# Performance work log

Measured on AMD Instinct MI355X. Metric: run time of the kernel, lower is better.

The kernel has to match this reference:

```python
import jax, jax.numpy as jnp
import numpy as np

C = 128
IC = C // 2  # inter_channels
EPS = 1e-5   # InstanceNorm2d default eps (affine=False -> no learned scale/shift)


def setup_inputs() -> dict:
    key = jax.random.key(0)
    ks = jax.random.split(key, 9)
    s = 0.05
    return {
        "x": jax.random.normal(ks[0], (4, C, 64, 64), dtype=jnp.float32),
        "g_w": jax.random.normal(ks[1], (IC, C), dtype=jnp.float32) * s,
        "g_b": jax.random.normal(ks[2], (IC,), dtype=jnp.float32) * s,
        "theta_w": jax.random.normal(ks[3], (IC, C), dtype=jnp.float32) * s,
        "theta_b": jax.random.normal(ks[4], (IC,), dtype=jnp.float32) * s,
        "phi_w": jax.random.normal(ks[5], (IC, C), dtype=jnp.float32) * s,
        "phi_b": jax.random.normal(ks[6], (IC,), dtype=jnp.float32) * s,
        "W_w": jax.random.normal(ks[7], (C, IC), dtype=jnp.float32) * s,
        "W_b": jax.random.normal(ks[8], (C,), dtype=jnp.float32) * s,
    }


def reference(x, g_w, g_b, theta_w, theta_b, phi_w, phi_b, W_w, W_b):
    B, Cc, H, Wd = x.shape
    N = H * Wd
    xf = x.reshape(B, Cc, N)  # [B, C, N]

    def proj(w, b):  # 1x1 conv == channel matmul
        return jnp.einsum('oc,bcn->bon', w, xf) + b[:, None]  # [B, IC, N]

    g_x = proj(g_w, g_b).transpose(0, 2, 1)        # [B, N, IC]
    theta_x = proj(theta_w, theta_b).transpose(0, 2, 1)  # [B, N, IC]
    phi_x = proj(phi_w, phi_b)                     # [B, IC, N]

    f = jnp.einsum('bnc,bcm->bnm', theta_x, phi_x)  # [B, N, N] unscaled affinity
    f = jax.nn.softmax(f, axis=-1)
    y = jnp.einsum('bnm,bmc->bnc', f, g_x)          # [B, N, IC]
    y = y.transpose(0, 2, 1)                        # [B, IC, N]

    W_y = jnp.einsum('oc,bcn->bon', W_w, y) + W_b[:, None]  # [B, C, N]
    # InstanceNorm2d (affine=False): normalize per (batch, channel) over spatial
    mean = W_y.mean(axis=-1, keepdims=True)
    var = W_y.var(axis=-1, keepdims=True)
    W_y = (W_y - mean) * jax.lax.rsqrt(var + EPS)

    return x + W_y.reshape(B, Cc, H, Wd)
```

## Files before the change

kernel.cpp:

```cpp
#include <hip/hip_runtime.h>

typedef __attribute__((ext_vector_type(4))) float f32x4;
typedef __attribute__((ext_vector_type(8))) short s16x8;
typedef __attribute__((ext_vector_type(4))) short s16x4;
typedef __attribute__((ext_vector_type(4))) unsigned int u32x4;

#define NB 4
#define CH 128
#define ICH 64
#define NSP 4096
#define KSPLIT 8
#define SEGK 512
#define LDK 72
#define LDW 136

static __device__ __forceinline__ unsigned short f2bf(float f) {
  unsigned int u = __builtin_bit_cast(unsigned int, f);
  u += 0x7fffu + ((u >> 16) & 1u);
  return (unsigned short)(u >> 16);
}

__global__ __launch_bounds__(256) void k_proj(
    const float* __restrict__ x,
    const float* __restrict__ gw, const float* __restrict__ gbias,
    const float* __restrict__ tw, const float* __restrict__ tbias,
    const float* __restrict__ pw, const float* __restrict__ pbias,
    unsigned short* __restrict__ thetaT, unsigned short* __restrict__ phiT,
    unsigned short* __restrict__ gout)
{
  __shared__ __align__(16) float sxf[CH * 65];
  __shared__ __align__(16) unsigned short sW[ICH * LDW];
  const int b = blockIdx.y, z = blockIdx.z;
  const int n0 = blockIdx.x * 64;
  const int t = threadIdx.x;
  const float* Wz = (z == 0) ? tw : (z == 1) ? pw : gw;
  const float* Bz = (z == 0) ? tbias : (z == 1) ? pbias : gbias;
  const float* xb = x + (size_t)b * CH * NSP;
#pragma unroll
  for (int i = 0; i < 8; ++i) {
    int idx = t + 256 * i;
    int c = idx >> 4, ch = idx & 15;
    *(float4*)(sxf + c * 65 + ch * 4) = *(const float4*)(xb + (size_t)c * NSP + n0 + ch * 4);
  }
#pragma unroll
  for (int i = 0; i < 8; ++i) {
    int idx = t + 256 * i;
    int o = idx >> 5, col = (idx & 31) * 4;
    float4 wv = *(const float4*)(Wz + o * CH + col);
    unsigned int p0 = (unsigned int)f2bf(wv.x) | ((unsigned int)f2bf(wv.y) << 16);
    unsigned int p1 = (unsigned int)f2bf(wv.z) | ((unsigned int)f2bf(wv.w) << 16);
    *(unsigned int*)(&sW[o * LDW + col]) = p0;
    *(unsigned int*)(&sW[o * LDW + col + 2]) = p1;
  }
  __syncthreads();

  const int wave = t >> 6, lane = t & 63;
  const int l15 = lane & 15, quad = lane >> 4;
  const int nw = wave * 16;
  s16x8 aq[4];
#pragma unroll
  for (int kc = 0; kc < 4; ++kc) {
#pragma unroll
    for (int j = 0; j < 8; ++j)
      aq[kc][j] = (short)f2bf(sxf[(kc * 32 + quad * 8 + j) * 65 + nw + l15]);
  }
  __syncthreads();

  unsigned short* ldsT = (unsigned short*)sxf;

#pragma unroll
  for (int osub = 0; osub < 4; ++osub) {
    f32x4 acc = (f32x4){0.f, 0.f, 0.f, 0.f};
#pragma unroll
    for (int kc = 0; kc < 4; ++kc) {
      const unsigned short* wp = &sW[(osub * 16 + l15) * LDW + kc * 32 + quad * 8];
      s16x4 lo = *(const s16x4*)(wp);
      s16x4 hi = *(const s16x4*)(wp + 4);
      s16x8 bw = __builtin_shufflevector(lo, hi, 0, 1, 2, 3, 4, 5, 6, 7);
      acc = __builtin_amdgcn_mfma_f32_16x16x32_bf16(aq[kc], bw, acc, 0, 0, 0);
    }
    float bv = Bz[osub * 16 + l15];
    if (z < 2) {
      unsigned short* outp = (z == 0) ? thetaT : phiT;
#pragma unroll
      for (int r = 0; r < 4; ++r)
        outp[((size_t)b * NSP + n0 + nw + quad * 4 + r) * ICH + osub * 16 + l15] =
            f2bf(acc[r] + bv);
    } else {
#pragma unroll
      for (int r = 0; r < 4; ++r)
        ldsT[(nw + quad * 4 + r) * LDK + osub * 16 + l15] = f2bf(acc[r] + bv);
    }
  }
  if (z == 2) {
    __syncthreads();
    int o = t >> 2, chunk = t & 3;
    unsigned short vv[16];
#pragma unroll
    for (int jj = 0; jj < 16; ++jj) vv[jj] = ldsT[(chunk * 16 + jj) * LDK + o];
    unsigned int words[8];
#pragma unroll
    for (int i = 0; i < 8; ++i)
      words[i] = (unsigned int)vv[2 * i] | ((unsigned int)vv[2 * i + 1] << 16);
    unsigned short* gp = gout + ((size_t)b * ICH + o) * NSP + n0 + chunk * 16;
    *(u32x4*)(gp) = (u32x4){words[0], words[1], words[2], words[3]};
    *(u32x4*)(gp + 8) = (u32x4){words[4], words[5], words[6], words[7]};
  }
}

__global__ __launch_bounds__(128, 2) void k_attn(
    const unsigned short* __restrict__ thetaT,
    const unsigned short* __restrict__ phiT,
    const unsigned short* __restrict__ gmat,
    float* __restrict__ Opart, float* __restrict__ lpart)
{
  __shared__ unsigned short ldsK[64 * LDK];
  __shared__ unsigned short ldsV[64 * LDK];
  __shared__ unsigned short ldsP[2][64 * LDK];
  const int qt = blockIdx.x, b = blockIdx.y, seg = blockIdx.z;
  const int t = threadIdx.x;
  const int wave = t >> 6, lane = t & 63;
  const int l15 = lane & 15, quad = lane >> 4;
  const int q0 = qt * 128 + wave * 64;

  s16x8 aq[4][2];
  const unsigned short* th = thetaT + ((size_t)b * NSP + q0) * ICH;
#pragma unroll
  for (int qs = 0; qs < 4; ++qs)
#pragma unroll
    for (int ks = 0; ks < 2; ++ks)
      aq[qs][ks] = __builtin_bit_cast(s16x8,
          *(const u32x4*)(th + (qs * 16 + l15) * ICH + ks * 32 + quad * 8));

  f32x4 Oacc[4][4];
  float lacc[4][4];
#pragma unroll
  for (int i = 0; i < 4; ++i)
#pragma unroll
    for (int j = 0; j < 4; ++j) { Oacc[i][j] = (f32x4){0.f, 0.f, 0.f, 0.f}; lacc[i][j] = 0.f; }

  const unsigned short* ph = phiT + (size_t)b * NSP * ICH;
  const unsigned short* gb = gmat + (size_t)b * ICH * NSP;
  const int k0 = seg * SEGK;

  for (int kt = 0; kt < SEGK / 64; ++kt) {
    const int key0 = k0 + kt * 64;
    __syncthreads();
#pragma unroll
    for (int i = 0; i < 4; ++i) {
      int idx = t + 128 * i;
      int row = idx >> 3, c16 = idx & 7;
      *(u32x4*)(&ldsK[row * LDK + c16 * 8]) =
          *(const u32x4*)(ph + (size_t)(key0 + row) * ICH + c16 * 8);
      *(u32x4*)(&ldsV[row * LDK + c16 * 8]) =
          *(const u32x4*)(gb + (size_t)row * NSP + key0 + c16 * 8);
    }
    __syncthreads();

    s16x8 bk[4][2];
#pragma unroll
    for (int kc = 0; kc < 4; ++kc)
#pragma unroll
      for (int ks = 0; ks < 2; ++ks)
        bk[kc][ks] = *(const s16x8*)(&ldsK[(kc * 16 + l15) * LDK + ks * 32 + quad * 8]);

    unsigned short* myP = &ldsP[wave][0];
#pragma unroll
    for (int qs = 0; qs < 4; ++qs) {
      f32x4 s[4];
#pragma unroll
      for (int kc = 0; kc < 4; ++kc) {
        f32x4 acc = (f32x4){0.f, 0.f, 0.f, 0.f};
        acc = __builtin_amdgcn_mfma_f32_16x16x32_bf16(aq[qs][0], bk[kc][0], acc, 0, 0, 0);
        acc = __builtin_amdgcn_mfma_f32_16x16x32_bf16(aq[qs][1], bk[kc][1], acc, 0, 0, 0);
        s[kc] = acc;
      }
      float tmp[4] = {0.f, 0.f, 0.f, 0.f};
#pragma unroll
      for (int kc = 0; kc < 4; ++kc)
#pragma unroll
        for (int r = 0; r < 4; ++r) {
          float e = __expf(s[kc][r]);
          s[kc][r] = e;
          tmp[r] += e;
        }
#pragma unroll
      for (int m = 1; m < 16; m <<= 1)
#pragma unroll
        for (int r = 0; r < 4; ++r) tmp[r] += __shfl_xor(tmp[r], m, 64);
#pragma unroll
      for (int r = 0; r < 4; ++r) lacc[qs][r] += tmp[r];
#pragma unroll
      for (int kc = 0; kc < 4; ++kc)
#pragma unroll
        for (int r = 0; r < 4; ++r)
          myP[(qs * 16 + quad * 4 + r) * LDK + kc * 16 + l15] = f2bf(s[kc][r]);
    }

    s16x8 bv[2][4];
#pragma unroll
    for (int ks = 0; ks < 2; ++ks)
#pragma unroll
      for (int ds = 0; ds < 4; ++ds)
        bv[ks][ds] = *(const s16x8*)(&ldsV[(ds * 16 + l15) * LDK + ks * 32 + quad * 8]);
#pragma unroll
    for (int qs = 0; qs < 4; ++qs)
#pragma unroll
      for (int ks = 0; ks < 2; ++ks) {
        s16x8 ap2 = *(const s16x8*)(&myP[(qs * 16 + l15) * LDK + ks * 32 + quad * 8]);
#pragma unroll
        for (int ds = 0; ds < 4; ++ds)
          Oacc[qs][ds] = __builtin_amdgcn_mfma_f32_16x16x32_bf16(ap2, bv[ks][ds], Oacc[qs][ds], 0, 0, 0);
      }
  }

  float* Ob = Opart + (((size_t)seg * NB + b) * NSP + q0) * ICH;
#pragma unroll
  for (int qs = 0; qs < 4; ++qs)
#pragma unroll
    for (int ds = 0; ds < 4; ++ds)
#pragma unroll
      for (int r = 0; r < 4; ++r)
        Ob[(qs * 16 + quad * 4 + r) * ICH + ds * 16 + l15] = Oacc[qs][ds][r];
  if (l15 == 0) {
    float* lb = lpart + ((size_t)seg * NB + b) * NSP + q0;
#pragma unroll
    for (int qs = 0; qs < 4; ++qs)
#pragma unroll
      for (int r = 0; r < 4; ++r)
        lb[qs * 16 + quad * 4 + r] = lacc[qs][r];
  }
}

__global__ __launch_bounds__(256) void k_combine(
    const float* __restrict__ Opart, const float* __restrict__ lpart,
    unsigned short* __restrict__ y)
{
  int idx = blockIdx.x * 256 + threadIdx.x;
  int d = idx & 63;
  int q = (idx >> 6) & (NSP - 1);
  int b = idx >> 18;
  float o = 0.f, l = 0.f;
#pragma unroll
  for (int s = 0; s < KSPLIT; ++s) {
    o += Opart[(((size_t)s * NB + b) * NSP + q) * ICH + d];
    l += lpart[((size_t)s * NB + b) * NSP + q];
  }
  y[idx] = f2bf(o / l);
}

__global__ __launch_bounds__(256) void k_wy(
    const unsigned short* __restrict__ y,
    const float* __restrict__ Ww,
    float* __restrict__ WyT, float* __restrict__ stat)
{
  const int b = blockIdx.y;
  const int nt = blockIdx.x;
  const int t = threadIdx.x;
  const int wave = t >> 6, lane = t & 63;
  const int l15 = lane & 15, quad = lane >> 4;
  s16x8 bw[8][2];
#pragma unroll
  for (int cc = 0; cc < 8; ++cc)
#pragma unroll
    for (int ks = 0; ks < 2; ++ks) {
      const float* wp = Ww + (cc * 16 + l15) * ICH + ks * 32 + quad * 8;
      s16x8 e;
#pragma unroll
      for (int j = 0; j < 8; ++j) e[j] = (short)f2bf(wp[j]);
      bw[cc][ks] = e;
    }
  float sums[8], sq[8];
#pragma unroll
  for (int cc = 0; cc < 8; ++cc) { sums[cc] = 0.f; sq[cc] = 0.f; }
  const unsigned short* yb = y + (size_t)b * NSP * ICH;
#pragma unroll
  for (int ns = 0; ns < 4; ++ns) {
    const int n0 = nt * 256 + wave * 64 + ns * 16;
    s16x8 ay[2];
#pragma unroll
    for (int ks = 0; ks < 2; ++ks)
      ay[ks] = __builtin_bit_cast(s16x8,
          *(const u32x4*)(yb + (size_t)(n0 + l15) * ICH + ks * 32 + quad * 8));
#pragma unroll
    for (int cc = 0; cc < 8; ++cc) {
      f32x4 acc = (f32x4){0.f, 0.f, 0.f, 0.f};
      acc = __builtin_amdgcn_mfma_f32_16x16x32_bf16(ay[0], bw[cc][0], acc, 0, 0, 0);
      acc = __builtin_amdgcn_mfma_f32_16x16x32_bf16(ay[1], bw[cc][1], acc, 0, 0, 0);
      float* wout = WyT + (size_t)(b * NSP + n0 + quad * 4) * CH + cc * 16 + l15;
#pragma unroll
      for (int r = 0; r < 4; ++r) {
        float v = acc[r];
        sums[cc] += v;
        sq[cc] += v * v;
        wout[r * CH] = v;
      }
    }
  }
#pragma unroll
  for (int cc = 0; cc < 8; ++cc) {
    sums[cc] += __shfl_xor(sums[cc], 16, 64);
    sums[cc] += __shfl_xor(sums[cc], 32, 64);
    sq[cc] += __shfl_xor(sq[cc], 16, 64);
    sq[cc] += __shfl_xor(sq[cc], 32, 64);
  }
  if (quad == 0) {
#pragma unroll
    for (int cc = 0; cc < 8; ++cc) {
      atomicAdd(&stat[(b * CH + cc * 16 + l15) * 2 + 0], sums[cc]);
      atomicAdd(&stat[(b * CH + cc * 16 + l15) * 2 + 1], sq[cc]);
    }
  }
}

__global__ __launch_bounds__(256) void k_norm(
    const float* __restrict__ WyT, const float* __restrict__ stat,
    const float* __restrict__ x, float* __restrict__ out)
{
  __shared__ float sWy[32 * 132];
  const int nt = blockIdx.x;
  const int b = blockIdx.y;
  const int t = threadIdx.x;
  const int n0 = nt * 32;
#pragma unroll
  for (int i = 0; i < 4; ++i) {
    int idx = t + 256 * i;
    int row = idx >> 5, c4 = idx & 31;
    *(float4*)(&sWy[row * 132 + c4 * 4]) =
        *(const float4*)(WyT + (size_t)(b * NSP + n0 + row) * CH + c4 * 4);
  }
  __syncthreads();
#pragma unroll
  for (int j = 0; j < 4; ++j) {
    int u = t + 256 * j;
    int co = u >> 3, nq = u & 7;
    float s = stat[(b * CH + co) * 2 + 0];
    float ss = stat[(b * CH + co) * 2 + 1];
    float mean = s * (1.f / NSP);
    float var = ss * (1.f / NSP) - mean * mean;
    float rs = rsqrtf(var + 1e-5f);
    float4 xv = *(const float4*)(x + (size_t)(b * CH + co) * NSP + n0 + nq * 4);
    float4 ov;
    ov.x = xv.x + (sWy[(nq * 4 + 0) * 132 + co] - mean) * rs;
    ov.y = xv.y + (sWy[(nq * 4 + 1) * 132 + co] - mean) * rs;
    ov.z = xv.z + (sWy[(nq * 4 + 2) * 132 + co] - mean) * rs;
    ov.w = xv.w + (sWy[(nq * 4 + 3) * 132 + co] - mean) * rs;
    *(float4*)(out + (size_t)(b * CH + co) * NSP + n0 + nq * 4) = ov;
  }
}

extern "C" void kernel_launch(void* const* d_in, const int* in_sizes, int n_in,
                              void* d_out, int out_size, void* d_ws, size_t ws_size,
                              hipStream_t stream)
{
  const float* x  = (const float*)d_in[0];
  const float* gw = (const float*)d_in[1];
  const float* gb = (const float*)d_in[2];
  const float* tw = (const float*)d_in[3];
  const float* tb = (const float*)d_in[4];
  const float* pw = (const float*)d_in[5];
  const float* pb = (const float*)d_in[6];
  const float* Ww = (const float*)d_in[7];
  float* out = (float*)d_out;
  char* ws = (char*)d_ws;
  unsigned short* thetaT = (unsigned short*)(ws);
  unsigned short* phiT   = (unsigned short*)(ws + (2ull << 20));
  unsigned short* gmat   = (unsigned short*)(ws + (4ull << 20));
  unsigned short* ybuf   = (unsigned short*)(ws + (6ull << 20));
  float* WyT   = (float*)(ws + (8ull << 20));
  float* stat  = (float*)(ws + (16ull << 20));
  float* Opart = (float*)(ws + (17ull << 20));
  float* lpart = (float*)(ws + (49ull << 20));

  hipMemsetAsync(stat, 0, NB * CH * 2 * sizeof(float), stream);
  k_proj<<<dim3(64, 4, 3), 256, 0, stream>>>(x, gw, gb, tw, tb, pw, pb, thetaT, phiT, gmat);
  k_attn<<<dim3(32, 4, 8), 128, 0, stream>>>(thetaT, phiT, gmat, Opart, lpart);
  k_combine<<<dim3((NB * NSP * ICH) / 256), 256, 0, stream>>>(Opart, lpart, ybuf);
  k_wy<<<dim3(16, 4), 256, 0, stream>>>(ybuf, Ww, WyT, stat);
  k_norm<<<dim3(128, 4), 256, 0, stream>>>(WyT, stat, x, out);
}
```

Baseline: 157.0 us.

## Fuse split-K combine into Wy projection, bf16 partials, exp2 softmax, MFMA row sums

Pre-scales theta by log2(e) so the attention kernel can use exp2f and convert P to bf16 by truncation. Row sums are computed with an MFMA against a ones vector instead of shuffle reductions. P is staged per 16-row slice. KSPLIT doubles to 16, blocks grow to 256 threads, and partial outputs are stored as bf16. The separate combine kernel is removed: k_wy now reduces the partials and normalises before its projection, which saves one launch and one round trip to memory, at the cost of extra precision loss and more split-K traffic.

```diff
diff --git a/kernel.cpp b/kernel.cpp
--- a/kernel.cpp
+++ b/kernel.cpp
@@ -1,4 +1,5 @@
 #include <hip/hip_runtime.h>
+#include <math.h>
 
 typedef __attribute__((ext_vector_type(4))) float f32x4;
 typedef __attribute__((ext_vector_type(8))) short s16x8;
@@ -9,8 +10,8 @@
 #define CH 128
 #define ICH 64
 #define NSP 4096
-#define KSPLIT 8
-#define SEGK 512
+#define KSPLIT 16
+#define SEGK (NSP / KSPLIT)
 #define LDK 72
 #define LDW 136
 
@@ -35,6 +36,7 @@
   const int t = threadIdx.x;
   const float* Wz = (z == 0) ? tw : (z == 1) ? pw : gw;
   const float* Bz = (z == 0) ? tbias : (z == 1) ? pbias : gbias;
+  const float scl = (z == 0) ? 1.44269504f : 1.0f;
   const float* xb = x + (size_t)b * CH * NSP;
 #pragma unroll
   for (int i = 0; i < 8; ++i) {
@@ -85,7 +87,7 @@
 #pragma unroll
       for (int r = 0; r < 4; ++r)
         outp[((size_t)b * NSP + n0 + nw + quad * 4 + r) * ICH + osub * 16 + l15] =
-            f2bf(acc[r] + bv);
+            f2bf((acc[r] + bv) * scl);
     } else {
 #pragma unroll
       for (int r = 0; r < 4; ++r)
@@ -108,20 +110,20 @@
   }
 }
 
-__global__ __launch_bounds__(128, 2) void k_attn(
+__global__ __launch_bounds__(256, 3) void k_attn(
     const unsigned short* __restrict__ thetaT,
     const unsigned short* __restrict__ phiT,
     const unsigned short* __restrict__ gmat,
-    float* __restrict__ Opart, float* __restrict__ lpart)
+    unsigned short* __restrict__ Opart, float* __restrict__ lpart)
 {
   __shared__ unsigned short ldsK[64 * LDK];
   __shared__ unsigned short ldsV[64 * LDK];
-  __shared__ unsigned short ldsP[2][64 * LDK];
+  __shared__ unsigned short ldsP[4][16 * LDK];
   const int qt = blockIdx.x, b = blockIdx.y, seg = blockIdx.z;
   const int t = threadIdx.x;
   const int wave = t >> 6, lane = t & 63;
   const int l15 = lane & 15, quad = lane >> 4;
-  const int q0 = qt * 128 + wave * 64;
+  const int q0 = qt * 256 + wave * 64;
 
   s16x8 aq[4][2];
   const unsigned short* th = thetaT + ((size_t)b * NSP + q0) * ICH;
@@ -133,11 +135,20 @@
           *(const u32x4*)(th + (qs * 16 + l15) * ICH + ks * 32 + quad * 8));
 
   f32x4 Oacc[4][4];
-  float lacc[4][4];
-#pragma unroll
-  for (int i = 0; i < 4; ++i)
-#pragma unroll
-    for (int j = 0; j < 4; ++j) { Oacc[i][j] = (f32x4){0.f, 0.f, 0.f, 0.f}; lacc[i][j] = 0.f; }
+  f32x4 lacc[4];
+#pragma unroll
+  for (int i = 0; i < 4; ++i) {
+    lacc[i] = (f32x4){0.f, 0.f, 0.f, 0.f};
+#pragma unroll
+    for (int j = 0; j < 4; ++j) Oacc[i][j] = (f32x4){0.f, 0.f, 0.f, 0.f};
+  }
+
+  s16x8 bones;
+  {
+    short v = (l15 == 0) ? (short)0x3F80 : (short)0;
+#pragma unroll
+    for (int j = 0; j < 8; ++j) bones[j] = v;
+  }
 
   const unsigned short* ph = phiT + (size_t)b * NSP * ICH;
   const unsigned short* gb = gmat + (size_t)b * ICH * NSP;
@@ -148,12 +159,14 @@
     __syncthreads();
 #pragma unroll
     for (int i = 0; i < 4; ++i) {
-      int idx = t + 128 * i;
-      int row = idx >> 3, c16 = idx & 7;
-      *(u32x4*)(&ldsK[row * LDK + c16 * 8]) =
-          *(const u32x4*)(ph + (size_t)(key0 + row) * ICH + c16 * 8);
-      *(u32x4*)(&ldsV[row * LDK + c16 * 8]) =
-          *(const u32x4*)(gb + (size_t)row * NSP + key0 + c16 * 8);
+      int idx = t + 256 * i;
+      int rr = (idx >> 3) & 63, c8 = (idx & 7) * 8;
+      if (idx < 512)
+        *(u32x4*)(&ldsK[rr * LDK + c8]) =
+            *(const u32x4*)(ph + (size_t)(key0 + rr) * ICH + c8);
+      else
+        *(u32x4*)(&ldsV[rr * LDK + c8]) =
+            *(const u32x4*)(gb + (size_t)rr * NSP + key0 + c8);
     }
     __syncthreads();
 
@@ -163,65 +176,47 @@
 #pragma unroll
       for (int ks = 0; ks < 2; ++ks)
         bk[kc][ks] = *(const s16x8*)(&ldsK[(kc * 16 + l15) * LDK + ks * 32 + quad * 8]);
-
-    unsigned short* myP = &ldsP[wave][0];
-#pragma unroll
-    for (int qs = 0; qs < 4; ++qs) {
-      f32x4 s[4];
-#pragma unroll
-      for (int kc = 0; kc < 4; ++kc) {
-        f32x4 acc = (f32x4){0.f, 0.f, 0.f, 0.f};
-        acc = __builtin_amdgcn_mfma_f32_16x16x32_bf16(aq[qs][0], bk[kc][0], acc, 0, 0, 0);
-        acc = __builtin_amdgcn_mfma_f32_16x16x32_bf16(aq[qs][1], bk[kc][1], acc, 0, 0, 0);
-        s[kc] = acc;
-      }
-      float tmp[4] = {0.f, 0.f, 0.f, 0.f};
-#pragma unroll
-      for (int kc = 0; kc < 4; ++kc)
-#pragma unroll
-        for (int r = 0; r < 4; ++r) {
-          float e = __expf(s[kc][r]);
-          s[kc][r] = e;
-          tmp[r] += e;
-        }
-#pragma unroll
-      for (int m = 1; m < 16; m <<= 1)
-#pragma unroll
-        for (int r = 0; r < 4; ++r) tmp[r] += __shfl_xor(tmp[r], m, 64);
-#pragma unroll
-      for (int r = 0; r < 4; ++r) lacc[qs][r] += tmp[r];
-#pragma unroll
-      for (int kc = 0; kc < 4; ++kc)
-#pragma unroll
-        for (int r = 0; r < 4; ++r)
-          myP[(qs * 16 + quad * 4 + r) * LDK + kc * 16 + l15] = f2bf(s[kc][r]);
-    }
-
     s16x8 bv[2][4];
 #pragma unroll
     for (int ks = 0; ks < 2; ++ks)
 #pragma unroll
       for (int ds = 0; ds < 4; ++ds)
         bv[ks][ds] = *(const s16x8*)(&ldsV[(ds * 16 + l15) * LDK + ks * 32 + quad * 8]);
-#pragma unroll
-    for (int qs = 0; qs < 4; ++qs)
+
+    unsigned short* myP = &ldsP[wave][0];
+#pragma unroll
+    for (int qs = 0; qs < 4; ++qs) {
+#pragma unroll
+      for (int kc = 0; kc < 4; ++kc) {
+        f32x4 sacc = (f32x4){0.f, 0.f, 0.f, 0.f};
+        sacc = __builtin_amdgcn_mfma_f32_16x16x32_bf16(aq[qs][0], bk[kc][0], sacc, 0, 0, 0);
+        sacc = __builtin_amdgcn_mfma_f32_16x16x32_bf16(aq[qs][1], bk[kc][1], sacc, 0, 0, 0);
+#pragma unroll
+        for (int r = 0; r < 4; ++r) {
+          float e = exp2f(sacc[r]);
+          myP[(quad * 4 + r) * LDK + kc * 16 + l15] =
+              (unsigned short)(__builtin_bit_cast(unsigned int, e) >> 16);
+        }
+      }
 #pragma unroll
       for (int ks = 0; ks < 2; ++ks) {
-        s16x8 ap2 = *(const s16x8*)(&myP[(qs * 16 + l15) * LDK + ks * 32 + quad * 8]);
+        s16x8 ap = *(const s16x8*)(&myP[l15 * LDK + ks * 32 + quad * 8]);
+        lacc[qs] = __builtin_amdgcn_mfma_f32_16x16x32_bf16(ap, bones, lacc[qs], 0, 0, 0);
 #pragma unroll
         for (int ds = 0; ds < 4; ++ds)
-          Oacc[qs][ds] = __builtin_amdgcn_mfma_f32_16x16x32_bf16(ap2, bv[ks][ds], Oacc[qs][ds], 0, 0, 0);
+          Oacc[qs][ds] = __builtin_amdgcn_mfma_f32_16x16x32_bf16(ap, bv[ks][ds], Oacc[qs][ds], 0, 0, 0);
       }
-  }
-
-  float* Ob = Opart + (((size_t)seg * NB + b) * NSP + q0) * ICH;
+    }
+  }
+
+  unsigned short* Ob = Opart + (((size_t)seg * NB + b) * NSP + q0) * ICH;
 #pragma unroll
   for (int qs = 0; qs < 4; ++qs)
 #pragma unroll
     for (int ds = 0; ds < 4; ++ds)
 #pragma unroll
       for (int r = 0; r < 4; ++r)
-        Ob[(qs * 16 + quad * 4 + r) * ICH + ds * 16 + l15] = Oacc[qs][ds][r];
+        Ob[(qs * 16 + quad * 4 + r) * ICH + ds * 16 + l15] = f2bf(Oacc[qs][ds][r]);
   if (l15 == 0) {
     float* lb = lpart + ((size_t)seg * NB + b) * NSP + q0;
 #pragma unroll
@@ -232,33 +227,42 @@
   }
 }
 
-__global__ __launch_bounds__(256) void k_combine(
-    const float* __restrict__ Opart, const float* __restrict__ lpart,
-    unsigned short* __restrict__ y)
-{
-  int idx = blockIdx.x * 256 + threadIdx.x;
-  int d = idx & 63;
-  int q = (idx >> 6) & (NSP - 1);
-  int b = idx >> 18;
-  float o = 0.f, l = 0.f;
-#pragma unroll
-  for (int s = 0; s < KSPLIT; ++s) {
-    o += Opart[(((size_t)s * NB + b) * NSP + q) * ICH + d];
-    l += lpart[((size_t)s * NB + b) * NSP + q];
-  }
-  y[idx] = f2bf(o / l);
-}
-
 __global__ __launch_bounds__(256) void k_wy(
-    const unsigned short* __restrict__ y,
+    const unsigned short* __restrict__ Opart, const float* __restrict__ lpart,
     const float* __restrict__ Ww,
     float* __restrict__ WyT, float* __restrict__ stat)
 {
-  const int b = blockIdx.y;
-  const int nt = blockIdx.x;
+  const int b = blockIdx.y, nt = blockIdx.x;
   const int t = threadIdx.x;
   const int wave = t >> 6, lane = t & 63;
   const int l15 = lane & 15, quad = lane >> 4;
+  const int n0 = nt * 64 + wave * 16;
+  float ls = 0.f;
+#pragma unroll
+  for (int s = 0; s < KSPLIT; ++s)
+    ls += lpart[((size_t)s * NB + b) * NSP + n0 + l15];
+  float inv = 1.0f / ls;
+  s16x8 ay[2];
+#pragma unroll
+  for (int ks = 0; ks < 2; ++ks) {
+    float acc8[8];
+#pragma unroll
+    for (int j = 0; j < 8; ++j) acc8[j] = 0.f;
+#pragma unroll
+    for (int s = 0; s < KSPLIT; ++s) {
+      const unsigned short* op =
+          Opart + (((size_t)s * NB + b) * NSP + n0 + l15) * ICH + ks * 32 + quad * 8;
+      u32x4 raw = *(const u32x4*)op;
+#pragma unroll
+      for (int w2 = 0; w2 < 4; ++w2) {
+        unsigned int u = raw[w2];
+        acc8[2 * w2]     += __builtin_bit_cast(float, u << 16);
+        acc8[2 * w2 + 1] += __builtin_bit_cast(float, u & 0xFFFF0000u);
+      }
+    }
+#pragma unroll
+    for (int j = 0; j < 8; ++j) ay[ks][j] = (short)f2bf(acc8[j] * inv);
+  }
   s16x8 bw[8][2];
 #pragma unroll
   for (int cc = 0; cc < 8; ++cc)
@@ -273,28 +277,18 @@
   float sums[8], sq[8];
 #pragma unroll
   for (int cc = 0; cc < 8; ++cc) { sums[cc] = 0.f; sq[cc] = 0.f; }
-  const unsigned short* yb = y + (size_t)b * NSP * ICH;
-#pragma unroll
-  for (int ns = 0; ns < 4; ++ns) {
-    const int n0 = nt * 256 + wave * 64 + ns * 16;
-    s16x8 ay[2];
-#pragma unroll
-    for (int ks = 0; ks < 2; ++ks)
-      ay[ks] = __builtin_bit_cast(s16x8,
-          *(const u32x4*)(yb + (size_t)(n0 + l15) * ICH + ks * 32 + quad * 8));
-#pragma unroll
-    for (int cc = 0; cc < 8; ++cc) {
-      f32x4 acc = (f32x4){0.f, 0.f, 0.f, 0.f};
-      acc = __builtin_amdgcn_mfma_f32_16x16x32_bf16(ay[0], bw[cc][0], acc, 0, 0, 0);
-      acc = __builtin_amdgcn_mfma_f32_16x16x32_bf16(ay[1], bw[cc][1], acc, 0, 0, 0);
-      float* wout = WyT + (size_t)(b * NSP + n0 + quad * 4) * CH + cc * 16 + l15;
-#pragma unroll
-      for (int r = 0; r < 4; ++r) {
-        float v = acc[r];
-        sums[cc] += v;
-        sq[cc] += v * v;
-        wout[r * CH] = v;
-      }
+#pragma unroll
+  for (int cc = 0; cc < 8; ++cc) {
+    f32x4 acc = (f32x4){0.f, 0.f, 0.f, 0.f};
+    acc = __builtin_amdgcn_mfma_f32_16x16x32_bf16(ay[0], bw[cc][0], acc, 0, 0, 0);
+    acc = __builtin_amdgcn_mfma_f32_16x16x32_bf16(ay[1], bw[cc][1], acc, 0, 0, 0);
+    float* wout = WyT + ((size_t)b * NSP + n0 + quad * 4) * CH + cc * 16 + l15;
+#pragma unroll
+    for (int r = 0; r < 4; ++r) {
+      float v = acc[r];
+      sums[cc] += v;
+      sq[cc] += v * v;
+      wout[r * CH] = v;
     }
   }
 #pragma unroll
@@ -327,7 +321,7 @@
     int idx = t + 256 * i;
     int row = idx >> 5, c4 = idx & 31;
     *(float4*)(&sWy[row * 132 + c4 * 4]) =
-        *(const float4*)(WyT + (size_t)(b * NSP + n0 + row) * CH + c4 * 4);
+        *(const float4*)(WyT + ((size_t)b * NSP + n0 + row) * CH + c4 * 4);
   }
   __syncthreads();
 #pragma unroll
@@ -366,16 +360,14 @@
   unsigned short* thetaT = (unsigned short*)(ws);
   unsigned short* phiT   = (unsigned short*)(ws + (2ull << 20));
   unsigned short* gmat   = (unsigned short*)(ws + (4ull << 20));
-  unsigned short* ybuf   = (unsigned short*)(ws + (6ull << 20));
   float* WyT   = (float*)(ws + (8ull << 20));
   float* stat  = (float*)(ws + (16ull << 20));
-  float* Opart = (float*)(ws + (17ull << 20));
-  float* lpart = (float*)(ws + (49ull << 20));
+  float* lpart = (float*)(ws + (16ull << 20) + (1ull << 18));
+  unsigned short* Opart = (unsigned short*)(ws + (17ull << 20) + (1ull << 18));
 
   hipMemsetAsync(stat, 0, NB * CH * 2 * sizeof(float), stream);
   k_proj<<<dim3(64, 4, 3), 256, 0, stream>>>(x, gw, gb, tw, tb, pw, pb, thetaT, phiT, gmat);
-  k_attn<<<dim3(32, 4, 8), 128, 0, stream>>>(thetaT, phiT, gmat, Opart, lpart);
-  k_combine<<<dim3((NB * NSP * ICH) / 256), 256, 0, stream>>>(Opart, lpart, ybuf);
-  k_wy<<<dim3(16, 4), 256, 0, stream>>>(ybuf, Ww, WyT, stat);
+  k_attn<<<dim3(16, 4, KSPLIT), 256, 0, stream>>>(thetaT, phiT, gmat, Opart, lpart);
+  k_wy<<<dim3(64, 4), 256, 0, stream>>>(Opart, lpart, Ww, WyT, stat);
   k_norm<<<dim3(128, 4), 256, 0, stream>>>(WyT, stat, x, out);
 }
```

New measurement: 185.1 us. +17.9%, slower.
